# Kernel tuning notes

Hardware: AMD Instinct MI355X
Metric: run time of the kernel (lower is better)

## Reference

```python
import jax, jax.numpy as jnp
import numpy as np

N, E, H, C, L = 10000, 320000, 4, 128, 4  # nodes, edges, heads, hidden, gat layers
D_IN, E_DIM = 7, 5


def setup_inputs() -> dict:
    key = jax.random.key(0)
    ks = jax.random.split(key, 16)
    g = lambda i, shape, s=0.05: jax.random.normal(ks[i], shape, dtype=jnp.float32) * s
    z = lambda *s: jnp.zeros(s, jnp.float32)
    o = lambda *s: jnp.ones(s, jnp.float32)
    return {
        "x": g(0, (N, D_IN), 1.0),
        "edge_index": jax.random.randint(ks[1], (2, E), 0, N),
        "edge_attr": g(2, (E, E_DIM), 1.0),
        "emb_W": g(3, (D_IN, C)), "emb_b": z(C),
        "gat_Wl": g(4, (L, C, H * C)), "gat_Wr": g(5, (L, C, H * C)),
        "gat_We": g(6, (L, E_DIM, H * C)), "gat_att": g(7, (L, H, C)),
        "gat_b": z(L, C), "ln_g": o(L, C), "ln_b": z(L, C),
        "sp_W1": g(8, (2 * C, C)), "sp_b1": z(C),
        "sp_W2": g(9, (C, C)), "sp_b2": z(C),
        "sp_gW": g(10, (C, C)), "sp_gb": z(C),
        "fn_g": o(C), "fn_b": z(C),
    }


def _layernorm(x, g, b, eps=1e-5):
    m = x.mean(-1, keepdims=True)
    v = ((x - m) ** 2).mean(-1, keepdims=True)
    return (x - m) * jax.lax.rsqrt(v + eps) * g + b


def _gatv2(h, src, dst, edge_attr, Wl, Wr, We, att, b):
    # GATv2Conv(concat=False, edge_dim): x_j = Wl h[src], x_i = Wr h[dst]
    xl = (h @ Wl).reshape(-1, H, C)            # [N,H,C]
    xr = (h @ Wr).reshape(-1, H, C)            # [N,H,C]
    e = (edge_attr @ We).reshape(-1, H, C)      # [E,H,C]
    m = jax.nn.leaky_relu(xl[src] + xr[dst] + e, 0.2)
    logits = jnp.einsum('ehc,hc->eh', m, att)   # [E,H]
    mx = jax.ops.segment_max(logits, dst, num_segments=N)
    ex = jnp.exp(logits - mx[dst])
    den = jax.ops.segment_sum(ex, dst, num_segments=N)
    alpha = ex / den[dst]                       # softmax over incoming edges
    out = jax.ops.segment_sum(alpha[..., None] * xl[src], dst, num_segments=N)
    return out.mean(axis=1) + b                 # head-average (concat=False)


def _social_pool(h, src, dst, W1, b1, W2, b2, gW, gb):
    pair = jnp.concatenate([h[src], h[dst]], axis=-1)   # [E,2C]
    inter = jax.nn.relu(pair @ W1 + b1) @ W2 + b2       # [E,C]
    gated = inter * jax.nn.sigmoid(inter @ gW + gb)
    s = jax.ops.segment_sum(gated, src, num_segments=N)
    cnt = jax.ops.segment_sum(jnp.ones((src.shape[0],), h.dtype), src, num_segments=N)
    return s / jnp.maximum(cnt, 1.0)[:, None]           # scatter-mean


def reference(x, edge_index, edge_attr, emb_W, emb_b, gat_Wl, gat_Wr, gat_We,
              gat_att, gat_b, ln_g, ln_b, sp_W1, sp_b1, sp_W2, sp_b2,
              sp_gW, sp_gb, fn_g, fn_b):
    src, dst = edge_index[0], edge_index[1]
    h = jax.nn.relu(x @ emb_W + emb_b)
    for i in range(L):
        res = h
        h = _gatv2(h, src, dst, edge_attr, gat_Wl[i], gat_Wr[i], gat_We[i],
                   gat_att[i], gat_b[i])
        h = jax.nn.relu(h)
        h = _layernorm(h + res, ln_g[i], ln_b[i])
    h = h + _social_pool(h, src, dst, sp_W1, sp_b1, sp_W2, sp_b2, sp_gW, sp_gb)
    return _layernorm(h, fn_g, fn_b)
```

## Files before the change

kernel.cpp:

```cpp
#include <hip/hip_runtime.h>
#include <hip/hip_bf16.h>
#include <math.h>

#define N_NODES 10000
#define N_EDGES 320000
#define HEADS   4
#define CDIM    128
#define HC      512
#define LAYERS  4
#define DIN     7
#define EDIM    5

typedef short short8 __attribute__((ext_vector_type(8)));
typedef unsigned short us8 __attribute__((ext_vector_type(8)));
typedef float f32x4 __attribute__((ext_vector_type(4)));

__device__ __forceinline__ void atomAddF(float* p, float v) { unsafeAtomicAdd(p, v); }

__device__ __forceinline__ unsigned short f2bf(float f) {
  unsigned u = __float_as_uint(f);
  unsigned r = u + 0x7fffu + ((u >> 16) & 1u);
  return (unsigned short)(r >> 16);
}
__device__ __forceinline__ float bf2f(unsigned short u) {
  return __uint_as_float(((unsigned)u) << 16);
}

__global__ __launch_bounds__(256) void embed_kernel(
    const float* __restrict__ x, const float* __restrict__ W,
    const float* __restrict__ b, float* __restrict__ h, unsigned short* __restrict__ hbf)
{
  int t = blockIdx.x * 256 + threadIdx.x;
  int n = t >> 7, c = t & 127;
  float acc = b[c];
#pragma unroll
  for (int k = 0; k < DIN; ++k) acc += x[n * DIN + k] * W[k * CDIM + c];
  acc = fmaxf(acc, 0.f);
  h[t] = acc;
  hbf[t] = f2bf(acc);
}

__global__ __launch_bounds__(256) void pack_kernel(
    const float* __restrict__ Wl, const float* __restrict__ Wr,
    const float* __restrict__ W1, const float* __restrict__ W2,
    const float* __restrict__ gW, unsigned short* __restrict__ WlrT,
    unsigned short* __restrict__ W1T, unsigned short* __restrict__ W2T,
    unsigned short* __restrict__ gWT)
{
  int t = blockIdx.x * 256 + threadIdx.x;
  if (t < 524288) {
    int k = t & 127, n = (t >> 7) & 1023, l = t >> 17;
    float v = (n < 512) ? Wl[(size_t)(l * 128 + k) * 512 + n]
                        : Wr[(size_t)(l * 128 + k) * 512 + (n - 512)];
    WlrT[t] = f2bf(v);
  } else if (t < 524288 + 32768) {
    int u = t - 524288; int k = u & 127, n = u >> 7;
    float v = (n < 128) ? W1[k * 128 + n] : W1[(128 + k) * 128 + (n - 128)];
    W1T[u] = f2bf(v);
  } else if (t < 557056 + 16384) {
    int u = t - 557056; int k = u & 127, n = u >> 7;
    W2T[u] = f2bf(W2[k * 128 + n]);
  } else if (t < 573440 + 16384) {
    int u = t - 573440; int k = u & 127, n = u >> 7;
    gWT[u] = f2bf(gW[k * 128 + n]);
  }
}

__global__ __launch_bounds__(256) void hist_kernel(
    const int* __restrict__ ei, int* __restrict__ degD, int* __restrict__ degS)
{
  int e = blockIdx.x * 256 + threadIdx.x;
  if (e < N_EDGES) {
    atomicAdd(&degS[ei[e]], 1);
    atomicAdd(&degD[ei[N_EDGES + e]], 1);
  }
}

__global__ __launch_bounds__(1024) void scan_kernel(
    const int* __restrict__ degD, int* __restrict__ offD, int* __restrict__ curD,
    const int* __restrict__ degS, int* __restrict__ offS, int* __restrict__ curS, int n)
{
  __shared__ int wsum[16];
  __shared__ int carry;
  int tid = threadIdx.x, wid = tid >> 6, lane = tid & 63;
  for (int arr = 0; arr < 2; ++arr) {
    const int* deg = arr ? degS : degD;
    int* off = arr ? offS : offD;
    int* cur = arr ? curS : curD;
    if (tid == 0) carry = 0;
    __syncthreads();
    for (int base = 0; base < n; base += 1024) {
      int i = base + tid;
      int v = (i < n) ? deg[i] : 0;
      int incl = v;
#pragma unroll
      for (int o = 1; o < 64; o <<= 1) {
        int t2 = __shfl_up(incl, o);
        if (lane >= o) incl += t2;
      }
      if (lane == 63) wsum[wid] = incl;
      __syncthreads();
      if (tid < 16) {
        int wv = wsum[tid];
#pragma unroll
        for (int o = 1; o < 16; o <<= 1) {
          int t2 = __shfl_up(wv, o);
          if (tid >= o) wv += t2;
        }
        wsum[tid] = wv;
      }
      __syncthreads();
      int woff = (wid > 0) ? wsum[wid - 1] : 0;
      int excl = carry + woff + incl - v;
      if (i < n) { off[i] = excl; cur[i] = excl; }
      __syncthreads();
      if (tid == 0) carry += wsum[15];
      __syncthreads();
    }
    if (tid == 0) off[n] = carry;
    __syncthreads();
  }
}

__global__ __launch_bounds__(256) void scatter_kernel(
    const int* __restrict__ ei, int* __restrict__ curD, int* __restrict__ curS,
    int* __restrict__ eidD, int* __restrict__ eidS)
{
  int e = blockIdx.x * 256 + threadIdx.x;
  if (e < N_EDGES) {
    int s = ei[e], d = ei[N_EDGES + e];
    int p = atomicAdd(&curD[d], 1);
    eidD[p] = e;
    int q = atomicAdd(&curS[s], 1);
    eidS[q] = e;
  }
}

__global__ __launch_bounds__(256) void reorder_kernel(
    const int* __restrict__ ei, const float* __restrict__ eattr,
    const int* __restrict__ eidD, int* __restrict__ esrc,
    float4* __restrict__ ea4, float* __restrict__ ea1)
{
  int idx = blockIdx.x * 256 + threadIdx.x;
  if (idx < N_EDGES) {
    int e = eidD[idx];
    esrc[idx] = ei[e];
    const float* p = &eattr[(size_t)e * 5];
    ea4[idx] = make_float4(p[0], p[1], p[2], p[3]);
    ea1[idx] = p[4];
  }
}

__global__ __launch_bounds__(256) void mfma_gemm_kernel(
    const unsigned short* __restrict__ A, const unsigned short* __restrict__ BT,
    unsigned short* __restrict__ C, int M, int ldc)
{
  __shared__ __align__(16) unsigned short sA[64 * 128];
  __shared__ __align__(16) unsigned short sB[64 * 128];
  int tid = threadIdx.x;
  int bm = blockIdx.y * 64, bn = blockIdx.x * 64;
#pragma unroll
  for (int i = 0; i < 4; ++i) {
    int ch = tid + i * 256;
    int r = ch >> 4, kc = ch & 15;
    int gr = bm + r;
    short8 v = {0, 0, 0, 0, 0, 0, 0, 0};
    if (gr < M) v = *(const short8*)&A[(size_t)gr * 128 + kc * 8];
    *(short8*)&sA[r * 128 + ((kc ^ (r & 7)) * 8)] = v;
  }
#pragma unroll
  for (int i = 0; i < 4; ++i) {
    int ch = tid + i * 256;
    int r = ch >> 4, kc = ch & 15;
    short8 v = *(const short8*)&BT[(size_t)(bn + r) * 128 + kc * 8];
    *(short8*)&sB[r * 128 + ((kc ^ (r & 7)) * 8)] = v;
  }
  __syncthreads();
  int w = tid >> 6, lane = tid & 63;
  int wr = (w >> 1) * 32, wc = (w & 1) * 32;
  int l15 = lane & 15, q = lane >> 4;
  f32x4 acc00 = {0, 0, 0, 0}, acc01 = acc00, acc10 = acc00, acc11 = acc00;
#pragma unroll
  for (int ks = 0; ks < 4; ++ks) {
    int c0 = ks * 4 + q;
    int m0 = wr + l15, m1 = m0 + 16;
    int n0 = wc + l15, n1 = n0 + 16;
    short8 a0 = *(const short8*)&sA[m0 * 128 + ((c0 ^ (m0 & 7)) * 8)];
    short8 a1 = *(const short8*)&sA[m1 * 128 + ((c0 ^ (m1 & 7)) * 8)];
    short8 b0 = *(const short8*)&sB[n0 * 128 + ((c0 ^ (n0 & 7)) * 8)];
    short8 b1 = *(const short8*)&sB[n1 * 128 + ((c0 ^ (n1 & 7)) * 8)];
    acc00 = __builtin_amdgcn_mfma_f32_16x16x32_bf16(a0, b0, acc00, 0, 0, 0);
    acc01 = __builtin_amdgcn_mfma_f32_16x16x32_bf16(a0, b1, acc01, 0, 0, 0);
    acc10 = __builtin_amdgcn_mfma_f32_16x16x32_bf16(a1, b0, acc10, 0, 0, 0);
    acc11 = __builtin_amdgcn_mfma_f32_16x16x32_bf16(a1, b1, acc11, 0, 0, 0);
  }
#pragma unroll
  for (int mf = 0; mf < 2; ++mf) {
#pragma unroll
    for (int nf = 0; nf < 2; ++nf) {
      f32x4 acc = mf == 0 ? (nf == 0 ? acc00 : acc01) : (nf == 0 ? acc10 : acc11);
      int col = bn + wc + nf * 16 + l15;
#pragma unroll
      for (int r = 0; r < 4; ++r) {
        int row = bm + wr + mf * 16 + 4 * q + r;
        if (row < M) C[(size_t)row * ldc + col] = f2bf(acc[r]);
      }
    }
  }
}

__global__ __launch_bounds__(256) void gat_agg_kernel(
    const float* __restrict__ h_in, float* __restrict__ h_out,
    unsigned short* __restrict__ hbf_out, const unsigned short* __restrict__ xlr,
    const int* __restrict__ esrc, const float4* __restrict__ ea4,
    const float* __restrict__ ea1, const int* __restrict__ offD,
    const float* __restrict__ We, const float* __restrict__ att,
    const float* __restrict__ gbias, const float* __restrict__ lng,
    const float* __restrict__ lnb)
{
  int tid = threadIdx.x;
  int w = tid >> 6, lane = tid & 63;
  int n = blockIdx.x * 4 + w;
  int base = lane * 8;

  float wWe[5][8];
#pragma unroll
  for (int k = 0; k < 5; ++k) {
    float4 a = *(const float4*)&We[k * HC + base];
    float4 b = *(const float4*)&We[k * HC + base + 4];
    wWe[k][0] = a.x; wWe[k][1] = a.y; wWe[k][2] = a.z; wWe[k][3] = a.w;
    wWe[k][4] = b.x; wWe[k][5] = b.y; wWe[k][6] = b.z; wWe[k][7] = b.w;
  }
  float wAtt[8];
  {
    float4 a = *(const float4*)&att[base];
    float4 b = *(const float4*)&att[base + 4];
    wAtt[0] = a.x; wAtt[1] = a.y; wAtt[2] = a.z; wAtt[3] = a.w;
    wAtt[4] = b.x; wAtt[5] = b.y; wAtt[6] = b.z; wAtt[7] = b.w;
  }
  float xr_reg[8];
  {
    us8 u = *(const us8*)&xlr[(size_t)n * 1024 + 512 + base];
#pragma unroll
    for (int j = 0; j < 8; ++j) xr_reg[j] = bf2f(u[j]);
  }

  int e0 = offD[n], e1 = offD[n + 1];
  float m = -INFINITY, dsum = 0.f;
  float acc[8] = {0.f, 0.f, 0.f, 0.f, 0.f, 0.f, 0.f, 0.f};

  us8 uA = {0, 0, 0, 0, 0, 0, 0, 0}, uB = uA;
  float4 qaA = {0, 0, 0, 0}, qaB = {0, 0, 0, 0};
  float qeA = 0.f, qeB = 0.f;
  int sA1 = 0, sB1 = 0;

  if (e0 < e1) {
    int iB = (e0 + 1 < e1) ? e0 + 1 : e0;
    int sA0 = esrc[e0], sB0 = esrc[iB];
    uA = *(const us8*)&xlr[(size_t)sA0 * 1024 + base];
    uB = *(const us8*)&xlr[(size_t)sB0 * 1024 + base];
    qaA = ea4[e0]; qeA = ea1[e0];
    qaB = ea4[iB]; qeB = ea1[iB];
    int jA = (e0 + 2 < e1) ? e0 + 2 : e0;
    int jB = (e0 + 3 < e1) ? e0 + 3 : e0;
    sA1 = esrc[jA]; sB1 = esrc[jB];
  }

  for (int i = e0; i < e1; i += 2) {
    float x0[8], x1[8];
#pragma unroll
    for (int j = 0; j < 8; ++j) { x0[j] = bf2f(uA[j]); x1[j] = bf2f(uB[j]); }
    float a0 = qaA.x, a1 = qaA.y, a2 = qaA.z, a3 = qaA.w, a4 = qeA;
    float b0 = qaB.x, b1 = qaB.y, b2 = qaB.z, b3 = qaB.w, b4 = qeB;

    uA = *(const us8*)&xlr[(size_t)sA1 * 1024 + base];
    uB = *(const us8*)&xlr[(size_t)sB1 * 1024 + base];
    {
      int jA = (i + 2 < e1) ? i + 2 : e0;
      int jB = (i + 3 < e1) ? i + 3 : e0;
      qaA = ea4[jA]; qeA = ea1[jA];
      qaB = ea4[jB]; qeB = ea1[jB];
      int kA = (i + 4 < e1) ? i + 4 : e0;
      int kB = (i + 5 < e1) ? i + 5 : e0;
      sA1 = esrc[kA]; sB1 = esrc[kB];
    }

    float lg0 = 0.f, lg1 = 0.f;
#pragma unroll
    for (int j = 0; j < 8; ++j) {
      float v0 = x0[j] + xr_reg[j] + a0 * wWe[0][j] + a1 * wWe[1][j]
               + a2 * wWe[2][j] + a3 * wWe[3][j] + a4 * wWe[4][j];
      v0 = (v0 > 0.f) ? v0 : 0.2f * v0;
      lg0 += v0 * wAtt[j];
      float v1 = x1[j] + xr_reg[j] + b0 * wWe[0][j] + b1 * wWe[1][j]
               + b2 * wWe[2][j] + b3 * wWe[3][j] + b4 * wWe[4][j];
      v1 = (v1 > 0.f) ? v1 : 0.2f * v1;
      lg1 += v1 * wAtt[j];
    }
    lg0 += __shfl_xor(lg0, 1); lg1 += __shfl_xor(lg1, 1);
    lg0 += __shfl_xor(lg0, 2); lg1 += __shfl_xor(lg1, 2);
    lg0 += __shfl_xor(lg0, 4); lg1 += __shfl_xor(lg1, 4);
    lg0 += __shfl_xor(lg0, 8); lg1 += __shfl_xor(lg1, 8);
    lg1 = (i + 1 < e1) ? lg1 : -INFINITY;

    float nm = fmaxf(m, fmaxf(lg0, lg1));
    float sc = __expf(m - nm);
    float p0 = __expf(lg0 - nm);
    float p1 = __expf(lg1 - nm);
    dsum = dsum * sc + p0 + p1;
#pragma unroll
    for (int j = 0; j < 8; ++j) acc[j] = (acc[j] * sc + p0 * x0[j]) + p1 * x1[j];
    m = nm;
  }

  float inv = (dsum > 0.f) ? (1.f / dsum) : 0.f;
  int c8 = (lane & 15) * 8;
  float o[8];
  float s1 = 0.f, s2 = 0.f;
#pragma unroll
  for (int j = 0; j < 8; ++j) {
    float v = acc[j] * inv;
    v += __shfl_xor(v, 16);
    v += __shfl_xor(v, 32);
    float oo = 0.25f * v + gbias[c8 + j];
    oo = fmaxf(oo, 0.f);
    oo += h_in[(size_t)n * 128 + c8 + j];
    o[j] = oo;
    s1 += oo; s2 += oo * oo;
  }
  s1 += __shfl_xor(s1, 1);  s2 += __shfl_xor(s2, 1);
  s1 += __shfl_xor(s1, 2);  s2 += __shfl_xor(s2, 2);
  s1 += __shfl_xor(s1, 4);  s2 += __shfl_xor(s2, 4);
  s1 += __shfl_xor(s1, 8);  s2 += __shfl_xor(s2, 8);
  s1 += __shfl_xor(s1, 16); s2 += __shfl_xor(s2, 16);
  s1 += __shfl_xor(s1, 32); s2 += __shfl_xor(s2, 32);
  float mean = s1 * (1.f / 512.f);
  float var = s2 * (1.f / 512.f) - mean * mean;
  float rs = rsqrtf(var + 1e-5f);
  if (lane < 16) {
#pragma unroll
    for (int j = 0; j < 8; ++j) {
      float val = (o[j] - mean) * rs * lng[c8 + j] + lnb[c8 + j];
      h_out[(size_t)n * 128 + c8 + j] = val;
      hbf_out[(size_t)n * 128 + c8 + j] = f2bf(val);
    }
  }
}

__global__ __launch_bounds__(256) void sp_edge_kernel(
    const unsigned short* __restrict__ sab, const float* __restrict__ b1,
    const unsigned short* __restrict__ W2T, const float* __restrict__ b2,
    const unsigned short* __restrict__ gWT, const float* __restrict__ gb,
    const int* __restrict__ ei, const int* __restrict__ eidS,
    float* __restrict__ pool)
{
  __shared__ __align__(16) unsigned short sT[64 * 128];
  __shared__ __align__(16) float sU[128 * 65];
  __shared__ int rsrc[64];
  __shared__ int rdst[64];
  unsigned short* sB = (unsigned short*)sU;
  int tid = threadIdx.x;
  int ebase = blockIdx.x * 64;
  if (tid < 64) {
    int idx = ebase + tid;
    int s = -1, d = 0;
    if (idx < N_EDGES) { int e = eidS[idx]; s = ei[e]; d = ei[N_EDGES + e]; }
    rsrc[tid] = s; rdst[tid] = d;
  }
  __syncthreads();

#pragma unroll
  for (int i = 0; i < 4; ++i) {
    int ch = tid + i * 256;
    int r = ch >> 4, kc = ch & 15, c0 = kc * 8;
    int s = rsrc[r];
    short8 o = {0, 0, 0, 0, 0, 0, 0, 0};
    if (s >= 0) {
      int d = rdst[r];
      us8 ua = *(const us8*)&sab[(size_t)s * 256 + c0];
      us8 ub = *(const us8*)&sab[(size_t)d * 256 + 128 + c0];
      float4 bb0 = *(const float4*)&b1[c0];
      float4 bb1 = *(const float4*)&b1[c0 + 4];
      float bv[8] = {bb0.x, bb0.y, bb0.z, bb0.w, bb1.x, bb1.y, bb1.z, bb1.w};
#pragma unroll
      for (int j = 0; j < 8; ++j)
        o[j] = (short)f2bf(fmaxf(bf2f(ua[j]) + bf2f(ub[j]) + bv[j], 0.f));
    }
    *(short8*)&sT[r * 128 + ((kc ^ (r & 7)) * 8)] = o;
  }
#pragma unroll
  for (int i = 0; i < 8; ++i) {
    int ch = tid + i * 256;
    int n = ch >> 4, kc = ch & 15;
    short8 v = *(const short8*)&W2T[(size_t)n * 128 + kc * 8];
    *(short8*)&sB[n * 128 + ((kc ^ (n & 7)) * 8)] = v;
  }
  __syncthreads();

  int w = tid >> 6, lane = tid & 63;
  int r0 = w * 16;
  int l15 = lane & 15, q = lane >> 4;

  f32x4 acc1[8], acc2[8];
#pragma unroll
  for (int i = 0; i < 8; ++i) { acc1[i] = (f32x4){0, 0, 0, 0}; acc2[i] = acc1[i]; }
  {
    short8 a[4];
#pragma unroll
    for (int ks = 0; ks < 4; ++ks) {
      int m = r0 + l15;
      a[ks] = *(const short8*)&sT[m * 128 + (((ks * 4 + q) ^ (m & 7)) * 8)];
    }
#pragma unroll
    for (int nf = 0; nf < 8; ++nf) {
      int n = nf * 16 + l15;
#pragma unroll
      for (int ks = 0; ks < 4; ++ks) {
        short8 b = *(const short8*)&sB[n * 128 + (((ks * 4 + q) ^ (n & 7)) * 8)];
        acc1[nf] = __builtin_amdgcn_mfma_f32_16x16x32_bf16(a[ks], b, acc1[nf], 0, 0, 0);
      }
    }
  }
#pragma unroll
  for (int nf = 0; nf < 8; ++nf) {
    float bias = b2[nf * 16 + l15];
#pragma unroll
    for (int r = 0; r < 4; ++r) acc1[nf][r] += bias;
  }
  __syncthreads();

#pragma unroll
  for (int nf = 0; nf < 8; ++nf) {
    int colN = nf * 16 + l15;
    int kc = colN >> 3, j = colN & 7;
#pragma unroll
    for (int r = 0; r < 4; ++r) {
      int row = r0 + 4 * q + r;
      sT[row * 128 + ((kc ^ (row & 7)) * 8) + j] = f2bf(acc1[nf][r]);
    }
  }
#pragma unroll
  for (int i = 0; i < 8; ++i) {
    int ch = tid + i * 256;
    int n = ch >> 4, kc = ch & 15;
    short8 v = *(const short8*)&gWT[(size_t)n * 128 + kc * 8];
    *(short8*)&sB[n * 128 + ((kc ^ (n & 7)) * 8)] = v;
  }
  __syncthreads();

  {
    short8 a[4];
#pragma unroll
    for (int ks = 0; ks < 4; ++ks) {
      int m = r0 + l15;
      a[ks] = *(const short8*)&sT[m * 128 + (((ks * 4 + q) ^ (m & 7)) * 8)];
    }
#pragma unroll
    for (int nf = 0; nf < 8; ++nf) {
      int n = nf * 16 + l15;
#pragma unroll
      for (int ks = 0; ks < 4; ++ks) {
        short8 b = *(const short8*)&sB[n * 128 + (((ks * 4 + q) ^ (n & 7)) * 8)];
        acc2[nf] = __builtin_amdgcn_mfma_f32_16x16x32_bf16(a[ks], b, acc2[nf], 0, 0, 0);
      }
    }
  }
  __syncthreads();

  float* gT = sU;
#pragma unroll
  for (int nf = 0; nf < 8; ++nf) {
    int colN = nf * 16 + l15;
    float gbias = gb[colN];
#pragma unroll
    for (int r = 0; r < 4; ++r) {
      float g = acc2[nf][r] + gbias;
      float gate = 1.f / (1.f + __expf(-g));
      int row = r0 + 4 * q + r;
      gT[colN * 65 + row] = acc1[nf][r] * gate;
    }
  }
  __syncthreads();

  {
    int c = tid & 127, half = tid >> 7;
    int rbeg = half * 32, rend = rbeg + 32;
    int curs = -1; float run = 0.f;
    for (int r = rbeg; r < rend; ++r) {
      int s = rsrc[r];
      if (s != curs) {
        if (curs >= 0) atomAddF(&pool[(size_t)curs * 128 + c], run);
        curs = s; run = 0.f;
      }
      if (s >= 0) run += gT[c * 65 + r];
    }
    if (curs >= 0) atomAddF(&pool[(size_t)curs * 128 + c], run);
  }
}

__global__ __launch_bounds__(256) void finalize_kernel(
    const float* __restrict__ h, const float* __restrict__ pool,
    const int* __restrict__ degS, const float* __restrict__ g,
    const float* __restrict__ b, float* __restrict__ out)
{
  int t = blockIdx.x * 256 + threadIdx.x;
  int n = t >> 6, lane = t & 63;
  if (n >= N_NODES) return;
  float cnt = fmaxf((float)degS[n], 1.f);
  float a = h[(size_t)n * 128 + lane] + pool[(size_t)n * 128 + lane] / cnt;
  float c2 = h[(size_t)n * 128 + 64 + lane] + pool[(size_t)n * 128 + 64 + lane] / cnt;
  float s = a + c2, s2 = a * a + c2 * c2;
#pragma unroll
  for (int o = 1; o < 64; o <<= 1) { s += __shfl_xor(s, o); s2 += __shfl_xor(s2, o); }
  float mean = s * (1.f / 128.f);
  float var = s2 * (1.f / 128.f) - mean * mean;
  float rs = rsqrtf(var + 1e-5f);
  out[(size_t)n * 128 + lane] = (a - mean) * rs * g[lane] + b[lane];
  out[(size_t)n * 128 + 64 + lane] = (c2 - mean) * rs * g[64 + lane] + b[64 + lane];
}

extern "C" void kernel_launch(void* const* d_in, const int* in_sizes, int n_in,
                              void* d_out, int out_size, void* d_ws, size_t ws_size,
                              hipStream_t stream) {
  (void)in_sizes; (void)n_in; (void)out_size; (void)ws_size;
  const float* x     = (const float*)d_in[0];
  const int*   ei    = (const int*)d_in[1];
  const float* eattr = (const float*)d_in[2];
  const float* embW  = (const float*)d_in[3];
  const float* embB  = (const float*)d_in[4];
  const float* gWl   = (const float*)d_in[5];
  const float* gWr   = (const float*)d_in[6];
  const float* gWe   = (const float*)d_in[7];
  const float* gAtt  = (const float*)d_in[8];
  const float* gB    = (const float*)d_in[9];
  const float* lnG   = (const float*)d_in[10];
  const float* lnB   = (const float*)d_in[11];
  const float* spW1  = (const float*)d_in[12];
  const float* spB1  = (const float*)d_in[13];
  const float* spW2  = (const float*)d_in[14];
  const float* spB2  = (const float*)d_in[15];
  const float* spGW  = (const float*)d_in[16];
  const float* spGB  = (const float*)d_in[17];
  const float* fnG   = (const float*)d_in[18];
  const float* fnB   = (const float*)d_in[19];
  float* out = (float*)d_out;

  char* ws = (char*)d_ws;
  size_t off = 0;
  auto alloc = [&](size_t bytes) {
    void* p = ws + off;
    off = (off + bytes + 255) & ~(size_t)255;
    return p;
  };
  float* hA   = (float*)alloc((size_t)N_NODES * 128 * 4);
  float* hB   = (float*)alloc((size_t)N_NODES * 128 * 4);
  unsigned short* hbfA = (unsigned short*)alloc((size_t)N_NODES * 128 * 2);
  unsigned short* hbfB = (unsigned short*)alloc((size_t)N_NODES * 128 * 2);
  unsigned short* xlr  = (unsigned short*)alloc((size_t)N_NODES * 1024 * 2);
  unsigned short* sab  = (unsigned short*)alloc((size_t)N_NODES * 256 * 2);
  float* pool = (float*)alloc((size_t)N_NODES * 128 * 4);
  unsigned short* WlrT = (unsigned short*)alloc((size_t)4 * 1024 * 128 * 2);
  unsigned short* W1T  = (unsigned short*)alloc((size_t)256 * 128 * 2);
  unsigned short* W2T  = (unsigned short*)alloc((size_t)128 * 128 * 2);
  unsigned short* gWT  = (unsigned short*)alloc((size_t)128 * 128 * 2);
  int* degD = (int*)alloc((size_t)N_NODES * 4);
  int* degS = (int*)alloc((size_t)N_NODES * 4);
  int* offD = (int*)alloc((size_t)(N_NODES + 1) * 4);
  int* offS = (int*)alloc((size_t)(N_NODES + 1) * 4);
  int* curD = (int*)alloc((size_t)N_NODES * 4);
  int* curS = (int*)alloc((size_t)N_NODES * 4);
  int* eidD = (int*)alloc((size_t)N_EDGES * 4);
  int* eidS = (int*)alloc((size_t)N_EDGES * 4);
  int* esrc = (int*)alloc((size_t)N_EDGES * 4);
  float4* ea4 = (float4*)alloc((size_t)N_EDGES * 16);
  float* ea1 = (float*)alloc((size_t)N_EDGES * 4);

  hipMemsetAsync(degD, 0, (size_t)N_NODES * 4, stream);
  hipMemsetAsync(degS, 0, (size_t)N_NODES * 4, stream);
  hipMemsetAsync(pool, 0, (size_t)N_NODES * 128 * 4, stream);

  pack_kernel<<<(589824 + 255) / 256, 256, 0, stream>>>(gWl, gWr, spW1, spW2, spGW,
                                                        WlrT, W1T, W2T, gWT);
  embed_kernel<<<(N_NODES * 128) / 256, 256, 0, stream>>>(x, embW, embB, hA, hbfA);
  hist_kernel<<<(N_EDGES + 255) / 256, 256, 0, stream>>>(ei, degD, degS);
  scan_kernel<<<1, 1024, 0, stream>>>(degD, offD, curD, degS, offS, curS, N_NODES);
  scatter_kernel<<<(N_EDGES + 255) / 256, 256, 0, stream>>>(ei, curD, curS, eidD, eidS);
  reorder_kernel<<<(N_EDGES + 255) / 256, 256, 0, stream>>>(ei, eattr, eidD, esrc, ea4, ea1);

  const int MB64 = (N_NODES + 63) / 64;
  float* hcur = hA; float* hnext = hB;
  unsigned short* hbcur = hbfA; unsigned short* hbnext = hbfB;
  for (int l = 0; l < LAYERS; ++l) {
    mfma_gemm_kernel<<<dim3(16, MB64), 256, 0, stream>>>(
        hbcur, WlrT + (size_t)l * 1024 * 128, xlr, N_NODES, 1024);
    gat_agg_kernel<<<(N_NODES + 3) / 4, 256, 0, stream>>>(hcur, hnext, hbnext, xlr,
                                                          esrc, ea4, ea1, offD,
                                                          gWe + (size_t)l * EDIM * HC,
                                                          gAtt + (size_t)l * HC,
                                                          gB + (size_t)l * 128,
                                                          lnG + (size_t)l * 128,
                                                          lnB + (size_t)l * 128);
    float* t1 = hcur; hcur = hnext; hnext = t1;
    unsigned short* t2 = hbcur; hbcur = hbnext; hbnext = t2;
  }
  mfma_gemm_kernel<<<dim3(4, MB64), 256, 0, stream>>>(hbcur, W1T, sab, N_NODES, 256);
  sp_edge_kernel<<<(N_EDGES + 63) / 64, 256, 0, stream>>>(sab, spB1, W2T, spB2, gWT,
                                                          spGB, ei, eidS, pool);
  finalize_kernel<<<(N_NODES + 3) / 4, 256, 0, stream>>>(hcur, pool, degS, fnG, fnB, out);
}
```

Baseline: 720.9 us.

## Fold gate GEMM into precomputed W2·gW product and restructure social-pool edge kernel

Precomputes F = W2·gW and a fused gate bias (b2·gW + gb), so the gate logits come straight from the ReLU hidden activations. The two edge-level GEMMs then run side by side instead of one after the other. The edge kernel now uses 512 threads, with each wave holding a 16-column slice of both weight matrices in registers, which removes the shared-memory weight staging, the intermediate bf16 round-trip and several barriers. The pooling step now does per-4-row run-length atomics instead of the 32-row transposed accumulation, so more atomics may be issued. The gate input is no longer rounded to bf16 before gW, which changes numerics slightly.

```diff
diff --git a/kernel.cpp b/kernel.cpp
--- a/kernel.cpp
+++ b/kernel.cpp
@@ -45,7 +45,7 @@
     const float* __restrict__ W1, const float* __restrict__ W2,
     const float* __restrict__ gW, unsigned short* __restrict__ WlrT,
     unsigned short* __restrict__ W1T, unsigned short* __restrict__ W2T,
-    unsigned short* __restrict__ gWT)
+    unsigned short* __restrict__ gWT, unsigned short* __restrict__ W2bf)
 {
   int t = blockIdx.x * 256 + threadIdx.x;
   if (t < 524288) {
@@ -63,7 +63,20 @@
   } else if (t < 573440 + 16384) {
     int u = t - 573440; int k = u & 127, n = u >> 7;
     gWT[u] = f2bf(gW[k * 128 + n]);
-  }
+  } else if (t < 589824 + 16384) {
+    int u = t - 589824;
+    W2bf[u] = f2bf(W2[u]);
+  }
+}
+
+__global__ __launch_bounds__(128) void fuse_bias_kernel(
+    const float* __restrict__ b2, const float* __restrict__ gW,
+    const float* __restrict__ gb, float* __restrict__ gbF)
+{
+  int n = threadIdx.x;
+  float s = gb[n];
+  for (int k = 0; k < 128; ++k) s += b2[k] * gW[k * 128 + n];
+  gbF[n] = s;
 }
 
 __global__ __launch_bounds__(256) void hist_kernel(
@@ -347,154 +360,83 @@
   }
 }
 
-__global__ __launch_bounds__(256) void sp_edge_kernel(
+__global__ __launch_bounds__(512) void sp_edge_kernel(
     const unsigned short* __restrict__ sab, const float* __restrict__ b1,
     const unsigned short* __restrict__ W2T, const float* __restrict__ b2,
-    const unsigned short* __restrict__ gWT, const float* __restrict__ gb,
+    const unsigned short* __restrict__ FT, const float* __restrict__ gbF,
     const int* __restrict__ ei, const int* __restrict__ eidS,
     float* __restrict__ pool)
 {
   __shared__ __align__(16) unsigned short sT[64 * 128];
-  __shared__ __align__(16) float sU[128 * 65];
   __shared__ int rsrc[64];
   __shared__ int rdst[64];
-  unsigned short* sB = (unsigned short*)sU;
   int tid = threadIdx.x;
+  int w = tid >> 6, lane = tid & 63;
+  int l15 = lane & 15, q = lane >> 4;
+  int col = w * 16 + l15;
+
+  short8 bW[4], bF[4];
+#pragma unroll
+  for (int ks = 0; ks < 4; ++ks) {
+    bW[ks] = *(const short8*)&W2T[(size_t)col * 128 + (ks * 4 + q) * 8];
+    bF[ks] = *(const short8*)&FT [(size_t)col * 128 + (ks * 4 + q) * 8];
+  }
+  float b2c = b2[col];
+  float gbc = gbF[col];
+
   int ebase = blockIdx.x * 64;
   if (tid < 64) {
-    int idx = ebase + tid;
-    int s = -1, d = 0;
-    if (idx < N_EDGES) { int e = eidS[idx]; s = ei[e]; d = ei[N_EDGES + e]; }
-    rsrc[tid] = s; rdst[tid] = d;
+    int e = eidS[ebase + tid];
+    rsrc[tid] = ei[e];
+    rdst[tid] = ei[N_EDGES + e];
   }
   __syncthreads();
 
 #pragma unroll
-  for (int i = 0; i < 4; ++i) {
-    int ch = tid + i * 256;
+  for (int i = 0; i < 2; ++i) {
+    int ch = tid + i * 512;
     int r = ch >> 4, kc = ch & 15, c0 = kc * 8;
-    int s = rsrc[r];
-    short8 o = {0, 0, 0, 0, 0, 0, 0, 0};
-    if (s >= 0) {
-      int d = rdst[r];
-      us8 ua = *(const us8*)&sab[(size_t)s * 256 + c0];
-      us8 ub = *(const us8*)&sab[(size_t)d * 256 + 128 + c0];
-      float4 bb0 = *(const float4*)&b1[c0];
-      float4 bb1 = *(const float4*)&b1[c0 + 4];
-      float bv[8] = {bb0.x, bb0.y, bb0.z, bb0.w, bb1.x, bb1.y, bb1.z, bb1.w};
-#pragma unroll
-      for (int j = 0; j < 8; ++j)
-        o[j] = (short)f2bf(fmaxf(bf2f(ua[j]) + bf2f(ub[j]) + bv[j], 0.f));
-    }
+    int s = rsrc[r], d = rdst[r];
+    us8 ua = *(const us8*)&sab[(size_t)s * 256 + c0];
+    us8 ub = *(const us8*)&sab[(size_t)d * 256 + 128 + c0];
+    float4 bb0 = *(const float4*)&b1[c0];
+    float4 bb1 = *(const float4*)&b1[c0 + 4];
+    float bv[8] = {bb0.x, bb0.y, bb0.z, bb0.w, bb1.x, bb1.y, bb1.z, bb1.w};
+    short8 o;
+#pragma unroll
+    for (int j = 0; j < 8; ++j)
+      o[j] = (short)f2bf(fmaxf(bf2f(ua[j]) + bf2f(ub[j]) + bv[j], 0.f));
     *(short8*)&sT[r * 128 + ((kc ^ (r & 7)) * 8)] = o;
   }
-#pragma unroll
-  for (int i = 0; i < 8; ++i) {
-    int ch = tid + i * 256;
-    int n = ch >> 4, kc = ch & 15;
-    short8 v = *(const short8*)&W2T[(size_t)n * 128 + kc * 8];
-    *(short8*)&sB[n * 128 + ((kc ^ (n & 7)) * 8)] = v;
-  }
   __syncthreads();
 
-  int w = tid >> 6, lane = tid & 63;
-  int r0 = w * 16;
-  int l15 = lane & 15, q = lane >> 4;
-
-  f32x4 acc1[8], acc2[8];
-#pragma unroll
-  for (int i = 0; i < 8; ++i) { acc1[i] = (f32x4){0, 0, 0, 0}; acc2[i] = acc1[i]; }
-  {
-    short8 a[4];
+#pragma unroll
+  for (int rg = 0; rg < 4; ++rg) {
+    int m = rg * 16 + l15;
+    f32x4 acc1 = {0, 0, 0, 0}, acc2 = {0, 0, 0, 0};
 #pragma unroll
     for (int ks = 0; ks < 4; ++ks) {
-      int m = r0 + l15;
-      a[ks] = *(const short8*)&sT[m * 128 + (((ks * 4 + q) ^ (m & 7)) * 8)];
-    }
-#pragma unroll
-    for (int nf = 0; nf < 8; ++nf) {
-      int n = nf * 16 + l15;
-#pragma unroll
-      for (int ks = 0; ks < 4; ++ks) {
-        short8 b = *(const short8*)&sB[n * 128 + (((ks * 4 + q) ^ (n & 7)) * 8)];
-        acc1[nf] = __builtin_amdgcn_mfma_f32_16x16x32_bf16(a[ks], b, acc1[nf], 0, 0, 0);
-      }
-    }
-  }
-#pragma unroll
-  for (int nf = 0; nf < 8; ++nf) {
-    float bias = b2[nf * 16 + l15];
-#pragma unroll
-    for (int r = 0; r < 4; ++r) acc1[nf][r] += bias;
-  }
-  __syncthreads();
-
-#pragma unroll
-  for (int nf = 0; nf < 8; ++nf) {
-    int colN = nf * 16 + l15;
-    int kc = colN >> 3, j = colN & 7;
+      short8 a = *(const short8*)&sT[m * 128 + (((ks * 4 + q) ^ (m & 7)) * 8)];
+      acc1 = __builtin_amdgcn_mfma_f32_16x16x32_bf16(a, bW[ks], acc1, 0, 0, 0);
+      acc2 = __builtin_amdgcn_mfma_f32_16x16x32_bf16(a, bF[ks], acc2, 0, 0, 0);
+    }
+    int rb = rg * 16 + 4 * q;
+    float g[4];
 #pragma unroll
     for (int r = 0; r < 4; ++r) {
-      int row = r0 + 4 * q + r;
-      sT[row * 128 + ((kc ^ (row & 7)) * 8) + j] = f2bf(acc1[nf][r]);
-    }
-  }
-#pragma unroll
-  for (int i = 0; i < 8; ++i) {
-    int ch = tid + i * 256;
-    int n = ch >> 4, kc = ch & 15;
-    short8 v = *(const short8*)&gWT[(size_t)n * 128 + kc * 8];
-    *(short8*)&sB[n * 128 + ((kc ^ (n & 7)) * 8)] = v;
-  }
-  __syncthreads();
-
-  {
-    short8 a[4];
-#pragma unroll
-    for (int ks = 0; ks < 4; ++ks) {
-      int m = r0 + l15;
-      a[ks] = *(const short8*)&sT[m * 128 + (((ks * 4 + q) ^ (m & 7)) * 8)];
-    }
-#pragma unroll
-    for (int nf = 0; nf < 8; ++nf) {
-      int n = nf * 16 + l15;
-#pragma unroll
-      for (int ks = 0; ks < 4; ++ks) {
-        short8 b = *(const short8*)&sB[n * 128 + (((ks * 4 + q) ^ (n & 7)) * 8)];
-        acc2[nf] = __builtin_amdgcn_mfma_f32_16x16x32_bf16(a[ks], b, acc2[nf], 0, 0, 0);
-      }
-    }
-  }
-  __syncthreads();
-
-  float* gT = sU;
-#pragma unroll
-  for (int nf = 0; nf < 8; ++nf) {
-    int colN = nf * 16 + l15;
-    float gbias = gb[colN];
-#pragma unroll
-    for (int r = 0; r < 4; ++r) {
-      float g = acc2[nf][r] + gbias;
-      float gate = 1.f / (1.f + __expf(-g));
-      int row = r0 + 4 * q + r;
-      gT[colN * 65 + row] = acc1[nf][r] * gate;
-    }
-  }
-  __syncthreads();
-
-  {
-    int c = tid & 127, half = tid >> 7;
-    int rbeg = half * 32, rend = rbeg + 32;
-    int curs = -1; float run = 0.f;
-    for (int r = rbeg; r < rend; ++r) {
-      int s = rsrc[r];
-      if (s != curs) {
-        if (curs >= 0) atomAddF(&pool[(size_t)curs * 128 + c], run);
-        curs = s; run = 0.f;
-      }
-      if (s >= 0) run += gT[c * 65 + r];
-    }
-    if (curs >= 0) atomAddF(&pool[(size_t)curs * 128 + c], run);
+      float inter = acc1[r] + b2c;
+      float gg = acc2[r] + gbc;
+      g[r] = inter * (1.f / (1.f + __expf(-gg)));
+    }
+    int s0 = rsrc[rb], s1 = rsrc[rb + 1], s2 = rsrc[rb + 2], s3 = rsrc[rb + 3];
+    float run = g[0]; int cur = s0;
+    if (s1 == cur) run += g[1];
+    else { atomAddF(&pool[(size_t)cur * 128 + col], run); cur = s1; run = g[1]; }
+    if (s2 == cur) run += g[2];
+    else { atomAddF(&pool[(size_t)cur * 128 + col], run); cur = s2; run = g[2]; }
+    if (s3 == cur) run += g[3];
+    else { atomAddF(&pool[(size_t)cur * 128 + col], run); cur = s3; run = g[3]; }
+    atomAddF(&pool[(size_t)cur * 128 + col], run);
   }
 }
 
@@ -563,6 +505,9 @@
   unsigned short* W1T  = (unsigned short*)alloc((size_t)256 * 128 * 2);
   unsigned short* W2T  = (unsigned short*)alloc((size_t)128 * 128 * 2);
   unsigned short* gWT  = (unsigned short*)alloc((size_t)128 * 128 * 2);
+  unsigned short* W2bf = (unsigned short*)alloc((size_t)128 * 128 * 2);
+  unsigned short* FT   = (unsigned short*)alloc((size_t)128 * 128 * 2);
+  float* gbF = (float*)alloc((size_t)128 * 4);
   int* degD = (int*)alloc((size_t)N_NODES * 4);
   int* degS = (int*)alloc((size_t)N_NODES * 4);
   int* offD = (int*)alloc((size_t)(N_NODES + 1) * 4);
@@ -579,8 +524,11 @@
   hipMemsetAsync(degS, 0, (size_t)N_NODES * 4, stream);
   hipMemsetAsync(pool, 0, (size_t)N_NODES * 128 * 4, stream);
 
-  pack_kernel<<<(589824 + 255) / 256, 256, 0, stream>>>(gWl, gWr, spW1, spW2, spGW,
-                                                        WlrT, W1T, W2T, gWT);
+  pack_kernel<<<(606208 + 255) / 256, 256, 0, stream>>>(gWl, gWr, spW1, spW2, spGW,
+                                                        WlrT, W1T, W2T, gWT, W2bf);
+  mfma_gemm_kernel<<<dim3(2, 2), 256, 0, stream>>>(gWT, W2bf, FT, 128, 128);
+  fuse_bias_kernel<<<1, 128, 0, stream>>>(spB2, spGW, spGB, gbF);
+
   embed_kernel<<<(N_NODES * 128) / 256, 256, 0, stream>>>(x, embW, embB, hA, hbfA);
   hist_kernel<<<(N_EDGES + 255) / 256, 256, 0, stream>>>(ei, degD, degS);
   scan_kernel<<<1, 1024, 0, stream>>>(degD, offD, curD, degS, offS, curS, N_NODES);
@@ -604,7 +552,7 @@
     unsigned short* t2 = hbcur; hbcur = hbnext; hbnext = t2;
   }
   mfma_gemm_kernel<<<dim3(4, MB64), 256, 0, stream>>>(hbcur, W1T, sab, N_NODES, 256);
-  sp_edge_kernel<<<(N_EDGES + 63) / 64, 256, 0, stream>>>(sab, spB1, W2T, spB2, gWT,
-                                                          spGB, ei, eidS, pool);
+  sp_edge_kernel<<<N_EDGES / 64, 512, 0, stream>>>(sab, spB1, W2T, spB2, FT, gbF,
+                                                   ei, eidS, pool);
   finalize_kernel<<<(N_NODES + 3) / 4, 256, 0, stream>>>(hcur, pool, degS, fnG, fnB, out);
 }
```

Result: slower. 757.7 us (+5.1%).
